# Performance work log

Measured on AMD Instinct MI355X. Metric: run time of the kernel, lower is better.

The kernel has to match this reference:

```python
import jax, jax.numpy as jnp
import numpy as np

D_MODEL = 1024
N_HEADS = 16
HEAD_DIM = D_MODEL // N_HEADS
B, L = 2, 2048


def setup_inputs() -> dict:
    key = jax.random.key(0)
    ks = jax.random.split(key, 12)
    s = 1.0 / np.sqrt(D_MODEL)
    inp = {
        'q': jax.random.normal(ks[0], (B, L, D_MODEL), dtype=jnp.float32),
        'k': jax.random.normal(ks[1], (B, L, D_MODEL), dtype=jnp.float32),
        'v': jax.random.normal(ks[2], (B, L, D_MODEL), dtype=jnp.float32),
        'Wq': jax.random.uniform(ks[3], (D_MODEL, D_MODEL), jnp.float32, -s, s),
        'bq': jax.random.uniform(ks[4], (D_MODEL,), jnp.float32, -s, s),
        'Wk': jax.random.uniform(ks[5], (D_MODEL, D_MODEL), jnp.float32, -s, s),
        'bk': jax.random.uniform(ks[6], (D_MODEL,), jnp.float32, -s, s),
        'Wv': jax.random.uniform(ks[7], (D_MODEL, D_MODEL), jnp.float32, -s, s),
        'bv': jax.random.uniform(ks[8], (D_MODEL,), jnp.float32, -s, s),
        'Wo': jax.random.uniform(ks[9], (D_MODEL, D_MODEL), jnp.float32, -s, s),
        'bo': jax.random.uniform(ks[10], (D_MODEL,), jnp.float32, -s, s),
    }
    return inp


def _heads(x):
    # (B, L, D) -> (B, H, L, Dh)
    b, l, _ = x.shape
    return x.reshape(b, l, N_HEADS, HEAD_DIM).transpose(0, 2, 1, 3)


def reference(q, k, v, Wq, bq, Wk, bk, Wv, bv, Wo, bo):
    # Linear projections (torch Linear: x @ W.T + b)
    qh = _heads(q @ Wq.T + bq)
    kh = _heads(k @ Wk.T + bk)
    vh = _heads(v @ Wv.T + bv)
    scale = 1.0 / jnp.sqrt(jnp.asarray(HEAD_DIM, dtype=qh.dtype))
    scores = jnp.einsum('bhqd,bhkd->bhqk', qh, kh) * scale  # (B,H,L,L)
    attn = jax.nn.softmax(scores, axis=-1)
    out = jnp.einsum('bhqk,bhkd->bhqd', attn, vh)
    out = out.transpose(0, 2, 1, 3).reshape(q.shape[0], q.shape[1], D_MODEL)
    return out @ Wo.T + bo
```

## Files before the change

kernel.cpp:

```cpp
#include <hip/hip_runtime.h>

typedef unsigned short u16;
typedef __bf16 bf16x8 __attribute__((ext_vector_type(8)));
typedef float f32x4 __attribute__((ext_vector_type(4)));
typedef float f32x16 __attribute__((ext_vector_type(16)));
typedef unsigned short u16x8 __attribute__((ext_vector_type(8)));
typedef unsigned int u32x2 __attribute__((ext_vector_type(2)));

#define LSEQ 2048
#define DM 1024
#define NH 16
#define HD 64
#define SCALE_Q 0.1803368801111244f

__device__ __forceinline__ u16 f2bf(float f) {
  union { float f; unsigned int u; } x;
  x.f = f;
  unsigned int u = x.u;
  u += 0x7FFFu + ((u >> 16) & 1u);
  return (u16)(u >> 16);
}

__device__ __forceinline__ float fexp2(float x) {
  return __builtin_amdgcn_exp2f(x);
}

__device__ __forceinline__ void async16(const void* g, void* l) {
  __builtin_amdgcn_global_load_lds(
      (const __attribute__((address_space(1))) void*)g,
      (__attribute__((address_space(3))) void*)l, 16, 0, 0);
}

__device__ __forceinline__ f32x4 mfma16(bf16x8 a, bf16x8 b, f32x4 c) {
  return __builtin_amdgcn_mfma_f32_16x16x32_bf16(a, b, c, 0, 0, 0);
}
__device__ __forceinline__ f32x16 mfma32(bf16x8 a, bf16x8 b, f32x16 c) {
  return __builtin_amdgcn_mfma_f32_32x32x16_bf16(a, b, c, 0, 0, 0);
}

__device__ __forceinline__ unsigned cvtpk(float lo, float hi) {
  unsigned r;
  asm("v_cvt_pk_bf16_f32 %0, %1, %2" : "=v"(r) : "v"(lo), "v"(hi));
  return r;
}
__device__ __forceinline__ void pswap(unsigned &a, unsigned &b) {
  asm("v_permlane32_swap_b32 %0, %1" : "+v"(a), "+v"(b));
}
__device__ __forceinline__ bf16x8 mk8(unsigned w0, unsigned w1, unsigned w2, unsigned w3) {
  union { unsigned u[4]; bf16x8 v; } x;
  x.u[0] = w0; x.u[1] = w1; x.u[2] = w2; x.u[3] = w3;
  return x.v;
}
__device__ __forceinline__ f32x16 zero16() {
  f32x16 z;
#pragma unroll
  for (int i = 0; i < 16; ++i) z[i] = 0.f;
  return z;
}

__global__ __launch_bounds__(256) void cvt7(
    const float* __restrict__ a0, const float* __restrict__ a1,
    const float* __restrict__ a2, const float* __restrict__ a3,
    const float* __restrict__ a4, const float* __restrict__ a5,
    const float* __restrict__ a6,
    u16* __restrict__ b0, u16* __restrict__ b1, u16* __restrict__ b2,
    u16* __restrict__ b3, u16* __restrict__ b4, u16* __restrict__ b5,
    u16* __restrict__ b6)
{
  const int t = blockIdx.y;
  const float* s; u16* d; int n;
  switch (t) {
    case 0: s = a0; d = b0; n = 1 << 22; break;
    case 1: s = a1; d = b1; n = 1 << 22; break;
    case 2: s = a2; d = b2; n = 1 << 22; break;
    case 3: s = a3; d = b3; n = 1 << 20; break;
    case 4: s = a4; d = b4; n = 1 << 20; break;
    case 5: s = a5; d = b5; n = 1 << 20; break;
    default: s = a6; d = b6; n = 1 << 20; break;
  }
  const int i = (blockIdx.x * 256 + threadIdx.x) * 8;
  if (i >= n) return;
  f32x4 f0 = *(const f32x4*)(s + i);
  f32x4 f1 = *(const f32x4*)(s + i + 4);
  u16x8 h;
#pragma unroll
  for (int j = 0; j < 4; ++j) { h[j] = f2bf(f0[j]); h[4 + j] = f2bf(f1[j]); }
  *(u16x8*)(d + i) = h;
}

__global__ __launch_bounds__(256) void gemm_qkv(
    const u16* __restrict__ Xq, const u16* __restrict__ Xk, const u16* __restrict__ Xv,
    const u16* __restrict__ Wqb, const u16* __restrict__ Wkb, const u16* __restrict__ Wvb,
    const float* __restrict__ bq, const float* __restrict__ bk, const float* __restrict__ bv,
    u16* __restrict__ Qp, u16* __restrict__ Kp, u16* __restrict__ Vt)
{
  __shared__ __align__(16) u16 As[2][64 * 32];
  __shared__ __align__(16) u16 Bs[2][128 * 32];

  const int tid = threadIdx.x;
  const int lane = tid & 63;
  const int wid = tid >> 6;
  const int lr = lane & 15, lg = lane >> 4;

  const int bm = blockIdx.x;
  const int by = blockIdx.y;
  const int wsel = by >> 3;
  const int bn = by & 7;

  const u16* A    = (wsel == 0) ? Xq  : (wsel == 1) ? Xk  : Xv;
  const u16* Bt   = (wsel == 0) ? Wqb : (wsel == 1) ? Wkb : Wvb;
  const float* bias = (wsel == 0) ? bq : (wsel == 1) ? bk : bv;

  const int r0 = tid >> 2;
  const int c0 = ((tid & 3) ^ ((r0 >> 1) & 3)) * 8;
  const size_t arow = (size_t)(bm * 64 + r0) * DM;
  const size_t brow0 = (size_t)(bn * 128 + r0) * DM;
  const size_t brow1 = (size_t)(bn * 128 + 64 + r0) * DM;

  const int sA = (lg ^ ((lr >> 1) & 3)) << 3;

#define GSTAGE(t, buf) do { \
    const int kk_ = (t) * 32; \
    async16(A + arow + kk_ + c0, &As[buf][tid * 8]); \
    async16(Bt + brow0 + kk_ + c0, &Bs[buf][tid * 8]); \
    async16(Bt + brow1 + kk_ + c0, &Bs[buf][2048 + tid * 8]); \
  } while (0)

  f32x4 acc[4][2];
#pragma unroll
  for (int m = 0; m < 4; ++m)
#pragma unroll
    for (int n = 0; n < 2; ++n) {
      f32x4 z = {0.f, 0.f, 0.f, 0.f};
      acc[m][n] = z;
    }

  GSTAGE(0, 0);
  __syncthreads();

  for (int kt = 0; kt < 32; ++kt) {
    const int cur = kt & 1, nxt = cur ^ 1;
    if (kt + 1 < 32) GSTAGE(kt + 1, nxt);
    bf16x8 af[4], bfr[2];
#pragma unroll
    for (int m = 0; m < 4; ++m)
      af[m] = *(const bf16x8*)&As[cur][(m * 16 + lr) * 32 + sA];
#pragma unroll
    for (int n = 0; n < 2; ++n)
      bfr[n] = *(const bf16x8*)&Bs[cur][(wid * 32 + n * 16 + lr) * 32 + sA];
#pragma unroll
    for (int m = 0; m < 4; ++m)
#pragma unroll
      for (int n = 0; n < 2; ++n)
        acc[m][n] = mfma16(af[m], bfr[n], acc[m][n]);
    __syncthreads();
  }
#undef GSTAGE

  if (wsel < 2) {
    u16* Out = (wsel == 0) ? Qp : Kp;
    const float oscale = (wsel == 0) ? SCALE_Q : 1.0f;
#pragma unroll
    for (int m = 0; m < 4; ++m) {
#pragma unroll
      for (int n = 0; n < 2; ++n) {
        const int col = bn * 128 + wid * 32 + n * 16 + lr;
        const float bv_ = bias[col];
        const int h = col >> 6, d = col & 63;
#pragma unroll
        for (int r = 0; r < 4; ++r) {
          const int row = bm * 64 + m * 16 + lg * 4 + r;
          const int b = row >> 11, l = row & 2047;
          Out[((size_t)(b * NH + h) * LSEQ + l) * HD + d] =
              f2bf((acc[m][n][r] + bv_) * oscale);
        }
      }
    }
  } else {
    const int b = (bm * 64) >> 11;
#pragma unroll
    for (int m = 0; m < 4; ++m) {
      const int l0 = (bm * 64 + m * 16 + lg * 4) & 2047;
#pragma unroll
      for (int n = 0; n < 2; ++n) {
        const int col = bn * 128 + wid * 32 + n * 16 + lr;
        const float bv_ = bias[col];
        const int h = col >> 6, d = col & 63;
        u32x2 w;
        w[0] = cvtpk(acc[m][n][0] + bv_, acc[m][n][1] + bv_);
        w[1] = cvtpk(acc[m][n][2] + bv_, acc[m][n][3] + bv_);
        *(u32x2*)&Vt[((size_t)(b * NH + h) * HD + d) * LSEQ + l0] = w;
      }
    }
  }
}

__global__ __launch_bounds__(256) void attn_fwd(
    const u16* __restrict__ Qp, const u16* __restrict__ Kp, const u16* __restrict__ Vt,
    u16* __restrict__ ctx)
{
  __shared__ __align__(16) u16 Ks[2][64 * 64];
  __shared__ __align__(16) u16 Vts[2][64 * 64];

  const int tid = threadIdx.x;
  const int wid = tid >> 6;
  const int lane = tid & 63;
  const int lq = lane & 31;
  const int h = lane >> 5;

  const int lid = blockIdx.x + (int)gridDim.x * blockIdx.y;
  const int xcd = lid & 7, slot = lid >> 3;
  const int bh = xcd * 4 + (slot >> 4);
  const int qt = slot & 15;

  const u16* Qb = Qp + (size_t)bh * (LSEQ * HD);
  const u16* Kb = Kp + (size_t)bh * (LSEQ * HD);
  const u16* Vb = Vt + (size_t)bh * (HD * LSEQ);

  const int q0 = qt * 128 + wid * 32;

  bf16x8 qf[4];
#pragma unroll
  for (int dk = 0; dk < 4; ++dk)
    qf[dk] = *(const bf16x8*)(Qb + (size_t)(q0 + lq) * HD + dk * 16 + h * 8);

  float l_run = 0.f;
  f32x16 o0 = zero16(), o1 = zero16();

  const int srow = tid >> 3;
  const int sslot = tid & 7;
  const int sswz = (sslot ^ (srow & 7)) << 3;
  const int ksrc = srow * 64 + sswz;
  const size_t vsrc0 = (size_t)srow * LSEQ + sswz;
  const size_t vsrc1 = (size_t)(srow + 32) * LSEQ + sswz;

#define ASTAGE(t, buf) do { \
    async16(Kb + (t) * 4096 + ksrc, &Ks[buf][tid * 8]); \
    async16(Kb + (t) * 4096 + 2048 + ksrc, &Ks[buf][2048 + tid * 8]); \
    async16(Vb + (t) * 64 + vsrc0, &Vts[buf][tid * 8]); \
    async16(Vb + (t) * 64 + vsrc1, &Vts[buf][2048 + tid * 8]); \
  } while (0)

  ASTAGE(0, 0);
  __syncthreads();

  for (int kt = 0; kt < LSEQ / 64; ++kt) {
    const int cur = kt & 1, nxt = cur ^ 1;
    if (kt + 1 < LSEQ / 64) ASTAGE(kt + 1, nxt);

    f32x16 st0 = zero16(), st1 = zero16();
    __builtin_amdgcn_s_setprio(1);
#pragma unroll
    for (int dk = 0; dk < 4; ++dk) {
      const int g = ((2 * dk + h) ^ (lq & 7)) << 3;
      bf16x8 kf0 = *(const bf16x8*)&Ks[cur][lq * 64 + g];
      bf16x8 kf1 = *(const bf16x8*)&Ks[cur][(32 + lq) * 64 + g];
      st0 = mfma32(kf0, qf[dk], st0);
      st1 = mfma32(kf1, qf[dk], st1);
    }
    __builtin_amdgcn_s_setprio(0);

    float rs = 0.f;
#pragma unroll
    for (int i = 0; i < 16; ++i) { st0[i] = fexp2(st0[i]); rs += st0[i]; }
#pragma unroll
    for (int i = 0; i < 16; ++i) { st1[i] = fexp2(st1[i]); rs += st1[i]; }
    l_run += rs;

    unsigned w[16];
#pragma unroll
    for (int m = 0; m < 4; ++m) {
      w[m * 2 + 0] = cvtpk(st0[4 * m + 0], st0[4 * m + 1]);
      w[m * 2 + 1] = cvtpk(st0[4 * m + 2], st0[4 * m + 3]);
      w[8 + m * 2 + 0] = cvtpk(st1[4 * m + 0], st1[4 * m + 1]);
      w[8 + m * 2 + 1] = cvtpk(st1[4 * m + 2], st1[4 * m + 3]);
    }
#pragma unroll
    for (int n = 0; n < 2; ++n) {
      pswap(w[n * 8 + 0], w[n * 8 + 2]);
      pswap(w[n * 8 + 1], w[n * 8 + 3]);
      pswap(w[n * 8 + 4], w[n * 8 + 6]);
      pswap(w[n * 8 + 5], w[n * 8 + 7]);
    }
    bf16x8 pa[4];
    pa[0] = mk8(w[0], w[1], w[2], w[3]);
    pa[1] = mk8(w[4], w[5], w[6], w[7]);
    pa[2] = mk8(w[8], w[9], w[10], w[11]);
    pa[3] = mk8(w[12], w[13], w[14], w[15]);

    __builtin_amdgcn_s_setprio(1);
#pragma unroll
    for (int ks = 0; ks < 4; ++ks) {
      const int g0g = ((2 * ks + h) ^ (lq & 7)) << 3;
      bf16x8 vf0 = *(const bf16x8*)&Vts[cur][lq * 64 + g0g];
      bf16x8 vf1 = *(const bf16x8*)&Vts[cur][(32 + lq) * 64 + g0g];
      o0 = mfma32(pa[ks], vf0, o0);
      o1 = mfma32(pa[ks], vf1, o1);
    }
    __builtin_amdgcn_s_setprio(0);

    __syncthreads();
  }
#undef ASTAGE

  const int b = bh >> 4, head = bh & 15;
  const float ltot = l_run + __shfl_xor(l_run, 32);
  const float linv = 1.0f / ltot;
#pragma unroll
  for (int reg = 0; reg < 16; ++reg) {
    const int row = (reg & 3) + 8 * (reg >> 2) + 4 * h;
    const float iv = __shfl(linv, row);
    const size_t base = ((size_t)(b * LSEQ + q0 + row)) * DM + head * HD;
    ctx[base + lq] = f2bf(o0[reg] * iv);
    ctx[base + 32 + lq] = f2bf(o1[reg] * iv);
  }
}

__global__ __launch_bounds__(256) void gemm_out(
    const u16* __restrict__ Actx, const u16* __restrict__ Wob,
    const float* __restrict__ bo, float* __restrict__ out)
{
  __shared__ __align__(16) u16 As[2][64 * 32];
  __shared__ __align__(16) u16 Bs[2][128 * 32];

  const int tid = threadIdx.x;
  const int lane = tid & 63;
  const int wid = tid >> 6;
  const int lr = lane & 15, lg = lane >> 4;

  const int bm = blockIdx.x;
  const int bn = blockIdx.y;

  const int r0 = tid >> 2;
  const int c0 = ((tid & 3) ^ ((r0 >> 1) & 3)) * 8;
  const size_t arow = (size_t)(bm * 64 + r0) * DM;
  const size_t brow0 = (size_t)(bn * 128 + r0) * DM;
  const size_t brow1 = (size_t)(bn * 128 + 64 + r0) * DM;

  const int sA = (lg ^ ((lr >> 1) & 3)) << 3;

#define GSTAGE(t, buf) do { \
    const int kk_ = (t) * 32; \
    async16(Actx + arow + kk_ + c0, &As[buf][tid * 8]); \
    async16(Wob + brow0 + kk_ + c0, &Bs[buf][tid * 8]); \
    async16(Wob + brow1 + kk_ + c0, &Bs[buf][2048 + tid * 8]); \
  } while (0)

  f32x4 acc[4][2];
#pragma unroll
  for (int m = 0; m < 4; ++m)
#pragma unroll
    for (int n = 0; n < 2; ++n) {
      f32x4 z = {0.f, 0.f, 0.f, 0.f};
      acc[m][n] = z;
    }

  GSTAGE(0, 0);
  __syncthreads();

  for (int kt = 0; kt < 32; ++kt) {
    const int cur = kt & 1, nxt = cur ^ 1;
    if (kt + 1 < 32) GSTAGE(kt + 1, nxt);
    bf16x8 af[4], bfr[2];
#pragma unroll
    for (int m = 0; m < 4; ++m)
      af[m] = *(const bf16x8*)&As[cur][(m * 16 + lr) * 32 + sA];
#pragma unroll
    for (int n = 0; n < 2; ++n)
      bfr[n] = *(const bf16x8*)&Bs[cur][(wid * 32 + n * 16 + lr) * 32 + sA];
#pragma unroll
    for (int m = 0; m < 4; ++m)
#pragma unroll
      for (int n = 0; n < 2; ++n)
        acc[m][n] = mfma16(af[m], bfr[n], acc[m][n]);
    __syncthreads();
  }
#undef GSTAGE

#pragma unroll
  for (int m = 0; m < 4; ++m) {
#pragma unroll
    for (int n = 0; n < 2; ++n) {
      const int col = bn * 128 + wid * 32 + n * 16 + lr;
      const float bv_ = bo[col];
#pragma unroll
      for (int r = 0; r < 4; ++r) {
        const int row = bm * 64 + m * 16 + lg * 4 + r;
        out[(size_t)row * DM + col] = acc[m][n][r] + bv_;
      }
    }
  }
}

extern "C" void kernel_launch(void* const* d_in, const int* in_sizes, int n_in,
                              void* d_out, int out_size, void* d_ws, size_t ws_size,
                              hipStream_t stream) {
  const float* q  = (const float*)d_in[0];
  const float* k  = (const float*)d_in[1];
  const float* v  = (const float*)d_in[2];
  const float* Wq = (const float*)d_in[3];
  const float* bq = (const float*)d_in[4];
  const float* Wk = (const float*)d_in[5];
  const float* bk = (const float*)d_in[6];
  const float* Wv = (const float*)d_in[7];
  const float* bv = (const float*)d_in[8];
  const float* Wo = (const float*)d_in[9];
  const float* bo = (const float*)d_in[10];
  float* out = (float*)d_out;

  u16* ws  = (u16*)d_ws;
  u16* Xqb = ws;
  u16* Xkb = Xqb + (4u << 20);
  u16* Xvb = Xkb + (4u << 20);
  u16* Wqb = Xvb + (4u << 20);
  u16* Wkb = Wqb + (1u << 20);
  u16* Wvb = Wkb + (1u << 20);
  u16* Wob = Wvb + (1u << 20);
  u16* Qp  = Wob + (1u << 20);
  u16* Kp  = Qp + (4u << 20);
  u16* Vt  = Kp + (4u << 20);
  u16* ctx = Xqb;

  cvt7<<<dim3(2048, 7), 256, 0, stream>>>(q, k, v, Wq, Wk, Wv, Wo,
                                          Xqb, Xkb, Xvb, Wqb, Wkb, Wvb, Wob);
  gemm_qkv<<<dim3(64, 24), 256, 0, stream>>>(Xqb, Xkb, Xvb, Wqb, Wkb, Wvb,
                                             bq, bk, bv, Qp, Kp, Vt);
  attn_fwd<<<dim3(16, 32), 256, 0, stream>>>(Qp, Kp, Vt, ctx);
  gemm_out<<<dim3(64, 8), 256, 0, stream>>>(ctx, Wob, bo, out);
}
```

Baseline: 138.9 us.

## Double attention KV tile to 128 keys and compute row sums via MFMA

The attention kernel now processes 128 keys per iteration instead of 64, doubling the K and V LDS tiles and halving the number of loop iterations and block-wide barriers. The softmax denominator, previously a VALU sum of exponentials plus shuffles, is now accumulated by an extra MFMA against a ones vector using the same bf16-rounded probabilities. This also makes the normalisation consistent with the bf16 P values. The cost is more LDS (64 KB per block), more registers for four score tiles, and one extra MFMA per k-step, which may reduce occupancy.

New measurement: 152.6 us. 9.9% more time.

```diff
diff --git a/kernel.cpp b/kernel.cpp
--- a/kernel.cpp
+++ b/kernel.cpp
@@ -199,8 +199,8 @@
     const u16* __restrict__ Qp, const u16* __restrict__ Kp, const u16* __restrict__ Vt,
     u16* __restrict__ ctx)
 {
-  __shared__ __align__(16) u16 Ks[2][64 * 64];
-  __shared__ __align__(16) u16 Vts[2][64 * 64];
+  __shared__ __align__(16) u16 Ks[2][128 * 64];
+  __shared__ __align__(16) u16 Vts[2][64 * 128];
 
   const int tid = threadIdx.x;
   const int wid = tid >> 6;
@@ -224,78 +224,93 @@
   for (int dk = 0; dk < 4; ++dk)
     qf[dk] = *(const bf16x8*)(Qb + (size_t)(q0 + lq) * HD + dk * 16 + h * 8);
 
-  float l_run = 0.f;
-  f32x16 o0 = zero16(), o1 = zero16();
+  const unsigned one2 = 0x3F803F80u;
+  const bf16x8 ones = mk8(one2, one2, one2, one2);
+
+  f32x16 o0 = zero16(), o1 = zero16(), lacc = zero16();
 
   const int srow = tid >> 3;
   const int sslot = tid & 7;
-  const int sswz = (sslot ^ (srow & 7)) << 3;
-  const int ksrc = srow * 64 + sswz;
-  const size_t vsrc0 = (size_t)srow * LSEQ + sswz;
-  const size_t vsrc1 = (size_t)(srow + 32) * LSEQ + sswz;
+  const int ksrc = srow * 64 + ((sslot ^ (srow & 7)) << 3);
+  const int vrow = tid >> 4;
+  const int vslot = tid & 15;
+  const int vswz = (vslot ^ vrow) << 3;
+  const size_t vsrc0 = (size_t)vrow * LSEQ + vswz;
+  const size_t vsrc1 = (size_t)(16 + vrow) * LSEQ + vswz;
+  const size_t vsrc2 = (size_t)(32 + vrow) * LSEQ + vswz;
+  const size_t vsrc3 = (size_t)(48 + vrow) * LSEQ + vswz;
 
 #define ASTAGE(t, buf) do { \
-    async16(Kb + (t) * 4096 + ksrc, &Ks[buf][tid * 8]); \
-    async16(Kb + (t) * 4096 + 2048 + ksrc, &Ks[buf][2048 + tid * 8]); \
-    async16(Vb + (t) * 64 + vsrc0, &Vts[buf][tid * 8]); \
-    async16(Vb + (t) * 64 + vsrc1, &Vts[buf][2048 + tid * 8]); \
+    const size_t kb_ = (size_t)(t) * 8192; \
+    async16(Kb + kb_ + ksrc, &Ks[buf][tid * 8]); \
+    async16(Kb + kb_ + 2048 + ksrc, &Ks[buf][2048 + tid * 8]); \
+    async16(Kb + kb_ + 4096 + ksrc, &Ks[buf][4096 + tid * 8]); \
+    async16(Kb + kb_ + 6144 + ksrc, &Ks[buf][6144 + tid * 8]); \
+    async16(Vb + (t) * 128 + vsrc0, &Vts[buf][tid * 8]); \
+    async16(Vb + (t) * 128 + vsrc1, &Vts[buf][2048 + tid * 8]); \
+    async16(Vb + (t) * 128 + vsrc2, &Vts[buf][4096 + tid * 8]); \
+    async16(Vb + (t) * 128 + vsrc3, &Vts[buf][6144 + tid * 8]); \
   } while (0)
 
   ASTAGE(0, 0);
   __syncthreads();
 
-  for (int kt = 0; kt < LSEQ / 64; ++kt) {
+  for (int kt = 0; kt < LSEQ / 128; ++kt) {
     const int cur = kt & 1, nxt = cur ^ 1;
-    if (kt + 1 < LSEQ / 64) ASTAGE(kt + 1, nxt);
-
-    f32x16 st0 = zero16(), st1 = zero16();
+    if (kt + 1 < LSEQ / 128) ASTAGE(kt + 1, nxt);
+
+    f32x16 st[4];
+#pragma unroll
+    for (int kb = 0; kb < 4; ++kb) st[kb] = zero16();
     __builtin_amdgcn_s_setprio(1);
 #pragma unroll
     for (int dk = 0; dk < 4; ++dk) {
-      const int g = ((2 * dk + h) ^ (lq & 7)) << 3;
-      bf16x8 kf0 = *(const bf16x8*)&Ks[cur][lq * 64 + g];
-      bf16x8 kf1 = *(const bf16x8*)&Ks[cur][(32 + lq) * 64 + g];
-      st0 = mfma32(kf0, qf[dk], st0);
-      st1 = mfma32(kf1, qf[dk], st1);
+      const int gk = ((2 * dk + h) ^ (lq & 7)) << 3;
+#pragma unroll
+      for (int kb = 0; kb < 4; ++kb) {
+        bf16x8 kf = *(const bf16x8*)&Ks[cur][(kb * 32 + lq) * 64 + gk];
+        st[kb] = mfma32(kf, qf[dk], st[kb]);
+      }
     }
     __builtin_amdgcn_s_setprio(0);
 
-    float rs = 0.f;
-#pragma unroll
-    for (int i = 0; i < 16; ++i) { st0[i] = fexp2(st0[i]); rs += st0[i]; }
-#pragma unroll
-    for (int i = 0; i < 16; ++i) { st1[i] = fexp2(st1[i]); rs += st1[i]; }
-    l_run += rs;
-
-    unsigned w[16];
-#pragma unroll
-    for (int m = 0; m < 4; ++m) {
-      w[m * 2 + 0] = cvtpk(st0[4 * m + 0], st0[4 * m + 1]);
-      w[m * 2 + 1] = cvtpk(st0[4 * m + 2], st0[4 * m + 3]);
-      w[8 + m * 2 + 0] = cvtpk(st1[4 * m + 0], st1[4 * m + 1]);
-      w[8 + m * 2 + 1] = cvtpk(st1[4 * m + 2], st1[4 * m + 3]);
-    }
-#pragma unroll
-    for (int n = 0; n < 2; ++n) {
-      pswap(w[n * 8 + 0], w[n * 8 + 2]);
-      pswap(w[n * 8 + 1], w[n * 8 + 3]);
-      pswap(w[n * 8 + 4], w[n * 8 + 6]);
-      pswap(w[n * 8 + 5], w[n * 8 + 7]);
-    }
-    bf16x8 pa[4];
-    pa[0] = mk8(w[0], w[1], w[2], w[3]);
-    pa[1] = mk8(w[4], w[5], w[6], w[7]);
-    pa[2] = mk8(w[8], w[9], w[10], w[11]);
-    pa[3] = mk8(w[12], w[13], w[14], w[15]);
+#pragma unroll
+    for (int kb = 0; kb < 4; ++kb)
+#pragma unroll
+      for (int i = 0; i < 16; ++i) st[kb][i] = fexp2(st[kb][i]);
+
+    unsigned w[32];
+#pragma unroll
+    for (int kb = 0; kb < 4; ++kb) {
+#pragma unroll
+      for (int m = 0; m < 4; ++m) {
+        w[kb * 8 + m * 2 + 0] = cvtpk(st[kb][4 * m + 0], st[kb][4 * m + 1]);
+        w[kb * 8 + m * 2 + 1] = cvtpk(st[kb][4 * m + 2], st[kb][4 * m + 3]);
+      }
+    }
+#pragma unroll
+    for (int kb = 0; kb < 4; ++kb) {
+      pswap(w[kb * 8 + 0], w[kb * 8 + 2]);
+      pswap(w[kb * 8 + 1], w[kb * 8 + 3]);
+      pswap(w[kb * 8 + 4], w[kb * 8 + 6]);
+      pswap(w[kb * 8 + 5], w[kb * 8 + 7]);
+    }
+    bf16x8 pa[8];
+#pragma unroll
+    for (int kb = 0; kb < 4; ++kb) {
+      pa[2 * kb + 0] = mk8(w[kb * 8 + 0], w[kb * 8 + 1], w[kb * 8 + 2], w[kb * 8 + 3]);
+      pa[2 * kb + 1] = mk8(w[kb * 8 + 4], w[kb * 8 + 5], w[kb * 8 + 6], w[kb * 8 + 7]);
+    }
 
     __builtin_amdgcn_s_setprio(1);
 #pragma unroll
-    for (int ks = 0; ks < 4; ++ks) {
-      const int g0g = ((2 * ks + h) ^ (lq & 7)) << 3;
-      bf16x8 vf0 = *(const bf16x8*)&Vts[cur][lq * 64 + g0g];
-      bf16x8 vf1 = *(const bf16x8*)&Vts[cur][(32 + lq) * 64 + g0g];
+    for (int ks = 0; ks < 8; ++ks) {
+      const int gv = ((2 * ks + h) ^ (lq & 15)) << 3;
+      bf16x8 vf0 = *(const bf16x8*)&Vts[cur][lq * 128 + gv];
+      bf16x8 vf1 = *(const bf16x8*)&Vts[cur][(32 + lq) * 128 + gv];
       o0 = mfma32(pa[ks], vf0, o0);
       o1 = mfma32(pa[ks], vf1, o1);
+      lacc = mfma32(pa[ks], ones, lacc);
     }
     __builtin_amdgcn_s_setprio(0);
 
@@ -304,12 +319,10 @@
 #undef ASTAGE
 
   const int b = bh >> 4, head = bh & 15;
-  const float ltot = l_run + __shfl_xor(l_run, 32);
-  const float linv = 1.0f / ltot;
 #pragma unroll
   for (int reg = 0; reg < 16; ++reg) {
     const int row = (reg & 3) + 8 * (reg >> 2) + 4 * h;
-    const float iv = __shfl(linv, row);
+    const float iv = 1.0f / lacc[reg];
     const size_t base = ((size_t)(b * LSEQ + q0 + row)) * DM + head * HD;
     ctx[base + lq] = f2bf(o0[reg] * iv);
     ctx[base + 32 + lq] = f2bf(o1[reg] * iv);
```
